# Kernel optimization log

Hardware: AMD Instinct MI355X
Metric: run time of the kernel (lower is better)

## Reference

```python
import jax, jax.numpy as jnp
import numpy as np

SEQ, B = 1024, 16384

def setup_inputs() -> dict:
    key = jax.random.key(0)
    ks = jax.random.split(key, 8)
    inputs = jax.random.normal(ks[0], (SEQ, B, 1), dtype=jnp.float32)
    returns = jax.random.uniform(ks[1], (SEQ - 1, B, 1), dtype=jnp.float32) * 0.02 - 0.01
    target = jax.random.uniform(ks[2], (1,), dtype=jnp.float32)  # pi_bar (no-trade region center)
    w_in = jax.random.normal(ks[3], (1, 1), dtype=jnp.float32)   # rnn.input_param.weight (1x1)
    w_h = jax.random.normal(ks[4], (1, 1), dtype=jnp.float32)    # rnn.hidden_param.weight (1x1)
    b_h = jax.random.normal(ks[5], (1, 1), dtype=jnp.float32)    # rnn.hidden_param.bias (1x1)
    w_fc1 = jax.random.normal(ks[6], (1, 1), dtype=jnp.float32)  # rnn.fc1_param.weight (1x1)
    w_fc2 = jax.random.normal(ks[7], (1, 1), dtype=jnp.float32)  # rnn.fc2_param.weight (1x1)
    return {"inputs": inputs, "returns": returns, "target": target,
            "w_in": w_in, "w_h": w_h, "b_h": b_h, "w_fc1": w_fc1, "w_fc2": w_fc2}


def reference(inputs, returns, target, w_in, w_h, b_h, w_fc1, w_fc2):
    # inputs: [S, B, 1], returns: [S-1, B, 1]; hidden_size == 1 so per-step state h: [B, 1]
    pi_bar = target[0]

    def step(h, xr):
        x, r = xr  # x: [B,1] input at step i, r: [B,1] return at step i-1
        # wealth renormalization of previous position
        h_adj = h * (1.0 + r) / (1.0 + h * r)
        # NoTradeRegionRNN.recurrence (all params are 1x1 -> scalar broadcasts)
        ingate = x @ w_in.T + w_h * h_adj - (pi_bar - b_h)
        ingate2 = w_fc1 * jax.nn.relu(ingate) + 2.0 * b_h
        h_new = w_fc2 * jax.nn.relu(ingate2) + pi_bar + b_h
        return h_new, h_new

    h0 = inputs[0]  # i==0: hidden = input[0] * ones -> just input[0], shape [B,1]
    hT, outs = jax.lax.scan(step, h0, (inputs[1:], returns))
    output = jnp.concatenate([h0[None], outs], axis=0)  # [S, B, 1]
    return output, hT
```

## Files before the change

### kernel.cpp

```cpp
#include <hip/hip_runtime.h>
#include <cstdint>


#define S_LEN 1024
#define B_LEN 16384
#define GSTEP ((size_t)4 * B_LEN)

typedef uint32_t u32x4 __attribute__((ext_vector_type(4)));
typedef float    f32x4 __attribute__((ext_vector_type(4)));
typedef float    f32x2 __attribute__((ext_vector_type(2)));

__device__ __forceinline__ u32x4 make_srsrc(const void* p) {
    u32x4 r;
    uint64_t a = (uint64_t)p;
    r.x = (uint32_t)a;
    r.y = (uint32_t)(a >> 32);
    r.z = 0xFFFFFFFFu;
    r.w = 0x00020000u;
    return r;
}

#define SBAR0 __builtin_amdgcn_sched_barrier(0)
#define WAITV(N) do { asm volatile("s_waitcnt vmcnt(%0)" :: "n"(N)); SBAR0; } while (0)
#define LGKMN(N) do { asm volatile("s_waitcnt lgkmcnt(%0)" :: "n"(N)); SBAR0; } while (0)

__device__ __forceinline__ void dma16(const float* g, float* l) {
    __builtin_amdgcn_global_load_lds(
        (const __attribute__((address_space(1))) void*)g,
        (__attribute__((address_space(3))) void*)l, 16, 0, 0);
}

__device__ __forceinline__ float step_fn(float h, float x, float r,
                                         float win, float wh,
                                         float c1, float c2, float c3,
                                         float wf1, float wf2) {
    float inv   = __builtin_amdgcn_rcpf(fmaf(h, r, 1.0f));
    float h_adj = fmaf(h, r, h) * inv;
    float ingate = fmaf(wh, h_adj, fmaf(x, win, c1));
    float t  = fmaxf(ingate, 0.0f);
    float g2 = fmaf(wf1, t, c2);
    float t2 = fmaxf(g2, 0.0f);
    return fmaf(wf2, t2, c3);
}

struct Consts { float winwf1, whwf1, c1wf1c2, c2p, wf2, c3; };

template<bool POS>
__device__ __forceinline__ void step_fast(float& st, float& hv,
                                          float x, float r, const Consts& C) {
    float A1 = C.wf2 * r;
    float B1 = C.c3 * r;
    float w  = fmaf(C.whwf1, r, C.whwf1);
    float A2 = C.wf2 * w;
    float B2 = C.c3 * w;
    float KK = fmaf(x, C.winwf1, C.c1wf1c2);
    float u  = fmaf(A1, st, B1);
    float M  = fmaf(A2, st, B2);
    float q  = fmaf(u, u, 1.0f);
    float om = 1.0f - u;
    float p  = om * q;
    float Aa = fmaf(M, p, KK);
    if (POS) st = fmaxf(Aa, C.c2p);
    else     st = fminf(fmaxf(Aa, 0.0f), C.c2p);
    hv = fmaf(C.wf2, st, C.c3);
}

template<bool POS>
__device__ __forceinline__ void step_first(float& st, float& hv,
                                           float x, float r, float h0,
                                           const Consts& C) {
    float w  = fmaf(C.whwf1, r, C.whwf1);
    float KK = fmaf(x, C.winwf1, C.c1wf1c2);
    float u  = h0 * r;
    float M  = w * h0;
    float q  = fmaf(u, u, 1.0f);
    float om = 1.0f - u;
    float p  = om * q;
    float Aa = fmaf(M, p, KK);
    if (POS) st = fmaxf(Aa, C.c2p);
    else     st = fminf(fmaxf(Aa, 0.0f), C.c2p);
    hv = fmaf(C.wf2, st, C.c3);
}

struct Bank { f32x2 x01, x23, r01, r23; };

#define RDG(g_, BK) do { \
    uint32_t ax_ = rbase + (uint32_t)(((g_) & 31) * 2048); \
    uint32_t ar_ = ax_ + 1024u; \
    asm volatile("ds_read2_b32 %0, %1 offset0:0 offset1:64"    : "=v"((BK).x01) : "v"(ax_)); \
    asm volatile("ds_read2_b32 %0, %1 offset0:128 offset1:192" : "=v"((BK).x23) : "v"(ax_)); \
    asm volatile("ds_read2_b32 %0, %1 offset0:0 offset1:64"    : "=v"((BK).r01) : "v"(ar_)); \
    asm volatile("ds_read2_b32 %0, %1 offset0:128 offset1:192" : "=v"((BK).r23) : "v"(ar_)); \
} while (0)

#define STEPS4B(BK) do { \
    step_fast<POS>(st, hv0, (BK).x01.x, (BK).r01.x, C); \
    step_fast<POS>(st, hv1, (BK).x01.y, (BK).r01.y, C); \
    step_fast<POS>(st, hv2, (BK).x23.x, (BK).r23.x, C); \
    step_fast<POS>(st, hv3, (BK).x23.y, (BK).r23.y, C); \
} while (0)

#define WRG(WA_) do { \
    asm volatile("ds_write2_b32 %0, %1, %2 offset0:0 offset1:64"    :: "v"(WA_), "v"(hv0), "v"(hv1)); \
    asm volatile("ds_write2_b32 %0, %1, %2 offset0:128 offset1:192" :: "v"(WA_), "v"(hv2), "v"(hv3)); \
} while (0)

#define PHASE(gr_, BKR, LGN_, BKC, WOFF_) do { \
    RDG(gr_, BKR); \
    LGKMN(LGN_); \
    STEPS4B(BKC); \
    { uint32_t wa_ = wb + (WOFF_); WRG(wa_); } \
} while (0)

template<bool POS>
__device__ __forceinline__ void wave0_impl(
    const float* inputs, const float* returns,
    float pi_bar, float win, float wh, float bh, float wf1, float wf2,
    float* out, int b0, int lane, float* ringp, float* outbp)
{
    const int b = b0 + lane;
    const float c1 = bh - pi_bar;
    const float c2 = 2.0f * bh;
    const float c3 = pi_bar + bh;
    Consts C;
    C.winwf1  = win * wf1;
    C.whwf1   = wh * wf1;
    C.c1wf1c2 = fmaf(c1, wf1, c2);
    C.c2p     = fmaxf(c2, 0.0f);
    C.wf2     = wf2;
    C.c3      = c3;

    const float h0v = inputs[b];
    out[b] = h0v;

    const uint32_t rbase = (uint32_t)(uintptr_t)ringp + (uint32_t)lane * 4u;
    const uint32_t wbase = (uint32_t)(uintptr_t)outbp + (uint32_t)lane * 4u;

    asm volatile("" ::: "memory");
    __builtin_amdgcn_s_barrier();

    Bank B0, B1, B2, B3;
    float st = 0.0f, hv0, hv1, hv2, hv3;

    RDG(0, B0);
    RDG(1, B1);
    LGKMN(0);

    for (int bt = 0; bt < 31; ++bt) {
        const int g0 = 8 * bt;
        const uint32_t wb = wbase + (uint32_t)((bt & 1) << 13);
        RDG(g0 + 2, B2);
        LGKMN(12);
        if (bt == 0) { step_first<POS>(st, hv0, B0.x01.x, B0.r01.x, h0v, C); }
        else         { step_fast<POS>(st, hv0, B0.x01.x, B0.r01.x, C); }
        step_fast<POS>(st, hv1, B0.x01.y, B0.r01.y, C);
        step_fast<POS>(st, hv2, B0.x23.x, B0.r23.x, C);
        step_fast<POS>(st, hv3, B0.x23.y, B0.r23.y, C);
        { uint32_t wa_ = wb; WRG(wa_); }
        PHASE(g0 + 3, B3, 10, B1, 1024);
        PHASE(g0 + 4, B0, 12, B2, 2048);
        PHASE(g0 + 5, B1, 12, B3, 3072);
        PHASE(g0 + 6, B2, 12, B0, 4096);
        PHASE(g0 + 7, B3, 12, B1, 5120);
        PHASE(g0 + 8, B0, 12, B2, 6144);
        LGKMN(8);
        STEPS4B(B3);
        { uint32_t wa_ = wb + 7168u; WRG(wa_); }
        RDG(g0 + 9, B1);
        LGKMN(4);
        __builtin_amdgcn_s_barrier();
    }

    {
        const uint32_t wb = wbase + 8192u;
        PHASE(250, B2, 12, B0, 0);
        PHASE(251, B3, 10, B1, 1024);
        PHASE(252, B0, 12, B2, 2048);
        PHASE(253, B1, 12, B3, 3072);
        PHASE(254, B2, 12, B0, 4096);
        PHASE(254, B3, 12, B1, 5120);
        LGKMN(8);
        STEPS4B(B2);
        { uint32_t wa_ = wb + 6144u; WRG(wa_); }
        LGKMN(0);
        __builtin_amdgcn_s_barrier();
    }

    asm volatile("" ::: "memory");

    float h = hv3;
#pragma unroll
    for (int s = 1021; s < S_LEN; ++s) {
        const float x = inputs[(size_t)s * B_LEN + b];
        const float r = returns[(size_t)(s - 1) * B_LEN + b];
        h = step_fn(h, x, r, win, wh, c1, c2, c3, wf1, wf2);
        out[(size_t)s * B_LEN + b] = h;
    }
    out[(size_t)S_LEN * B_LEN + b] = h;
}

#define DMA_GROUP() do { \
    float* lb_ = &ringf[(size_t)(dmag & 31) * 512]; \
    dma16(gxw, lb_); dma16(grw, lb_ + 256); \
    gxw += GSTEP; grw += GSTEP; ++dmag; \
} while (0)

#define WDR8(LOFF_, O0,O1,O2,O3,O4,O5,O6,O7) do { \
    uint32_t a_ = oa + (LOFF_); \
    asm volatile("ds_read_b128 %0, %1 offset:0"    : "=v"(O0) : "v"(a_)); \
    asm volatile("ds_read_b128 %0, %1 offset:1024" : "=v"(O1) : "v"(a_)); \
    asm volatile("ds_read_b128 %0, %1 offset:2048" : "=v"(O2) : "v"(a_)); \
    asm volatile("ds_read_b128 %0, %1 offset:3072" : "=v"(O3) : "v"(a_)); \
    asm volatile("ds_read_b128 %0, %1 offset:4096" : "=v"(O4) : "v"(a_)); \
    asm volatile("ds_read_b128 %0, %1 offset:5120" : "=v"(O5) : "v"(a_)); \
    asm volatile("ds_read_b128 %0, %1 offset:6144" : "=v"(O6) : "v"(a_)); \
    asm volatile("ds_read_b128 %0, %1 offset:7168" : "=v"(O7) : "v"(a_)); \
} while (0)

#define BST(O_) do { \
    asm volatile("buffer_store_dwordx4 %0, %1, %2, %3 offen" \
                 :: "v"(O_), "v"(vo), "s"(ro), "s"(so_)); \
    so_ += (4u << 16); \
} while (0)

#define W1_ITER(k_, LOFF_, NDMA_, PREN_, ENDN_, DOEND_, O0,O1,O2,O3,O4,O5,O6,O7) do { \
    __builtin_amdgcn_s_barrier(); \
    for (int gi_ = 0; gi_ < (NDMA_); ++gi_) { DMA_GROUP(); } \
    asm volatile("s_waitcnt vmcnt(%0)" :: "n"(PREN_)); SBAR0; \
    asm volatile("" :: "v"(O0),"v"(O1),"v"(O2),"v"(O3),"v"(O4),"v"(O5),"v"(O6),"v"(O7)); \
    WDR8(LOFF_, O0,O1,O2,O3,O4,O5,O6,O7); \
    LGKMN(0); \
    { uint32_t so_ = ((uint32_t)(32 * ((k_) - 1) + 1)) << 16; \
      BST(O0); BST(O1); BST(O2); BST(O3); BST(O4); BST(O5); BST(O6); BST(O7); } \
    if (DOEND_) { asm volatile("s_waitcnt vmcnt(%0)" :: "n"(ENDN_)); SBAR0; } \
} while (0)

__global__ __launch_bounds__(128) void wealth_rnn_kernel(
    const float* __restrict__ inputs,
    const float* __restrict__ returns,
    const float* __restrict__ target,
    const float* __restrict__ w_in_p,
    const float* __restrict__ w_h_p,
    const float* __restrict__ b_h_p,
    const float* __restrict__ w_fc1_p,
    const float* __restrict__ w_fc2_p,
    float* __restrict__ out)
{
    __shared__ float ringf[32 * 512];
    __shared__ float outbf[2 * 8 * 256];

    const int tid  = threadIdx.x;
    const int lane = tid & 63;
    const int wid  = tid >> 6;
    const int b0   = blockIdx.x * 64;

    if (wid == 0) {
        const float pi_bar = target[0];
        const float win = w_in_p[0];
        const float wh  = w_h_p[0];
        const float bh  = b_h_p[0];
        const float wf1 = w_fc1_p[0];
        const float wf2 = w_fc2_p[0];
        if (wf1 >= 0.0f)
            wave0_impl<true >(inputs, returns, pi_bar, win, wh, bh, wf1, wf2,
                              out, b0, lane, &ringf[0], &outbf[0]);
        else
            wave0_impl<false>(inputs, returns, pi_bar, win, wh, bh, wf1, wf2,
                              out, b0, lane, &ringf[0], &outbf[0]);
    } else {
        const int j = lane;
        u32x4 ro = make_srsrc(out);
        const uint32_t vo = (uint32_t)((((j >> 4) * B_LEN) + b0 + (j & 15) * 4) * 4);
        const uint32_t oa = (uint32_t)(uintptr_t)&outbf[0]
                            + (uint32_t)((j >> 4) * 256 + (j & 15) * 16);

        const int lr = j >> 4;
        const int lc = (j & 15) * 4;
        const float* gxw = inputs  + (size_t)(1 + lr) * B_LEN + b0 + lc;
        const float* grw = returns + (size_t)lr       * B_LEN + b0 + lc;
        int dmag = 0;

        for (int gi = 0; gi < 24; ++gi) { DMA_GROUP(); }
        WAITV(28);
        __builtin_amdgcn_s_barrier();

        for (int gi = 0; gi < 8; ++gi) { DMA_GROUP(); }
        WAITV(28);

        f32x4 o0={0,0,0,0},o1={0,0,0,0},o2={0,0,0,0},o3={0,0,0,0},
              o4={0,0,0,0},o5={0,0,0,0},o6={0,0,0,0},o7={0,0,0,0};
        f32x4 p0={0,0,0,0},p1={0,0,0,0},p2={0,0,0,0},p3={0,0,0,0},
              p4={0,0,0,0},p5={0,0,0,0},p6={0,0,0,0},p7={0,0,0,0};

        for (int k2 = 0; k2 < 13; ++k2) {
            const int k = 1 + 2 * k2;
            W1_ITER(k,     0,    8, 40, 36, 1, o0,o1,o2,o3,o4,o5,o6,o7);
            W1_ITER(k + 1, 8192, 8, 40, 36, 1, p0,p1,p2,p3,p4,p5,p6,p7);
        }
        W1_ITER(27, 0,    8, 40, 36, 1, o0,o1,o2,o3,o4,o5,o6,o7);
        W1_ITER(28, 8192, 7, 38, 34, 1, p0,p1,p2,p3,p4,p5,p6,p7);
        W1_ITER(29, 0,    0, 22, 18, 1, o0,o1,o2,o3,o4,o5,o6,o7);
        W1_ITER(30, 8192, 0,  8, 16, 1, p0,p1,p2,p3,p4,p5,p6,p7);
        W1_ITER(31, 0,    0,  8,  0, 0, o0,o1,o2,o3,o4,o5,o6,o7);
        __builtin_amdgcn_s_barrier();

        WAITV(8);
        asm volatile("" :: "v"(p0),"v"(p1),"v"(p2),"v"(p3),"v"(p4),"v"(p5),"v"(p6));
        {
            uint32_t a_ = oa + 8192u;
            asm volatile("ds_read_b128 %0, %1 offset:0"    : "=v"(p0) : "v"(a_));
            asm volatile("ds_read_b128 %0, %1 offset:1024" : "=v"(p1) : "v"(a_));
            asm volatile("ds_read_b128 %0, %1 offset:2048" : "=v"(p2) : "v"(a_));
            asm volatile("ds_read_b128 %0, %1 offset:3072" : "=v"(p3) : "v"(a_));
            asm volatile("ds_read_b128 %0, %1 offset:4096" : "=v"(p4) : "v"(a_));
            asm volatile("ds_read_b128 %0, %1 offset:5120" : "=v"(p5) : "v"(a_));
            asm volatile("ds_read_b128 %0, %1 offset:6144" : "=v"(p6) : "v"(a_));
        }
        LGKMN(0);
        {
            uint32_t so_ = ((uint32_t)993) << 16;
            BST(p0); BST(p1); BST(p2); BST(p3); BST(p4); BST(p5); BST(p6);
        }
    }
}

extern "C" void kernel_launch(void* const* d_in, const int* in_sizes, int n_in,
                              void* d_out, int out_size, void* d_ws, size_t ws_size,
                              hipStream_t stream) {
    const float* inputs  = (const float*)d_in[0];
    const float* returns = (const float*)d_in[1];
    const float* target  = (const float*)d_in[2];
    const float* w_in    = (const float*)d_in[3];
    const float* w_h     = (const float*)d_in[4];
    const float* b_h     = (const float*)d_in[5];
    const float* w_fc1   = (const float*)d_in[6];
    const float* w_fc2   = (const float*)d_in[7];
    float* out = (float*)d_out;

    dim3 grid(B_LEN / 64);
    dim3 block(128);
    hipLaunchKernelGGL(wealth_rnn_kernel, grid, block, 0, stream,
                       inputs, returns, target, w_in, w_h, b_h, w_fc1, w_fc2, out);
}
```

Baseline: 43.69 us.

## Store outputs directly from compute wave and enlarge LDS input ring

The compute wave now writes each step's hidden values straight to global memory with per-lane buffer_store_dword. It no longer stages them in an LDS output buffer for the helper wave to read back and store as dwordx4. The helper wave becomes a pure DMA producer, and the input ring grows from 32 to 64 groups with 16-step phases between barriers. The aim is to remove the LDS round trip and halve the barrier count. The cost is many narrower stores issued from the latency-critical serial wave, plus a larger LDS footprint.

```diff
diff --git a/kernel.cpp b/kernel.cpp
--- a/kernel.cpp
+++ b/kernel.cpp
@@ -7,7 +7,6 @@
 #define GSTEP ((size_t)4 * B_LEN)
 
 typedef uint32_t u32x4 __attribute__((ext_vector_type(4)));
-typedef float    f32x4 __attribute__((ext_vector_type(4)));
 typedef float    f32x2 __attribute__((ext_vector_type(2)));
 
 __device__ __forceinline__ u32x4 make_srsrc(const void* p) {
@@ -84,39 +83,37 @@
 
 struct Bank { f32x2 x01, x23, r01, r23; };
 
-#define RDG(g_, BK) do { \
-    uint32_t ax_ = rbase + (uint32_t)(((g_) & 31) * 2048); \
-    uint32_t ar_ = ax_ + 1024u; \
-    asm volatile("ds_read2_b32 %0, %1 offset0:0 offset1:64"    : "=v"((BK).x01) : "v"(ax_)); \
-    asm volatile("ds_read2_b32 %0, %1 offset0:128 offset1:192" : "=v"((BK).x23) : "v"(ax_)); \
+#define RDGA(AX_, BK) do { \
+    uint32_t ar_ = (AX_) + 1024u; \
+    asm volatile("ds_read2_b32 %0, %1 offset0:0 offset1:64"    : "=v"((BK).x01) : "v"(AX_)); \
+    asm volatile("ds_read2_b32 %0, %1 offset0:128 offset1:192" : "=v"((BK).x23) : "v"(AX_)); \
     asm volatile("ds_read2_b32 %0, %1 offset0:0 offset1:64"    : "=v"((BK).r01) : "v"(ar_)); \
     asm volatile("ds_read2_b32 %0, %1 offset0:128 offset1:192" : "=v"((BK).r23) : "v"(ar_)); \
 } while (0)
 
-#define STEPS4B(BK) do { \
-    step_fast<POS>(st, hv0, (BK).x01.x, (BK).r01.x, C); \
-    step_fast<POS>(st, hv1, (BK).x01.y, (BK).r01.y, C); \
-    step_fast<POS>(st, hv2, (BK).x23.x, (BK).r23.x, C); \
-    step_fast<POS>(st, hv3, (BK).x23.y, (BK).r23.y, C); \
-} while (0)
-
-#define WRG(WA_) do { \
-    asm volatile("ds_write2_b32 %0, %1, %2 offset0:0 offset1:64"    :: "v"(WA_), "v"(hv0), "v"(hv1)); \
-    asm volatile("ds_write2_b32 %0, %1, %2 offset0:128 offset1:192" :: "v"(WA_), "v"(hv2), "v"(hv3)); \
-} while (0)
-
-#define PHASE(gr_, BKR, LGN_, BKC, WOFF_) do { \
-    RDG(gr_, BKR); \
-    LGKMN(LGN_); \
-    STEPS4B(BKC); \
-    { uint32_t wa_ = wb + (WOFF_); WRG(wa_); } \
+#define BSTROW(HV_, ROWC_) do { \
+    uint32_t so_ = sob + (uint32_t)((ROWC_) << 16); \
+    asm volatile("buffer_store_dword %0, %1, %2, %3 offen" \
+                 :: "v"(HV_), "v"(voff), "s"(ro), "s"(so_)); \
+} while (0)
+
+#define PH(p_, BKR, BKC) do { \
+    int gr_ = g0 + (p_) + 2; if (gr_ > 254) gr_ = 254; \
+    { uint32_t ra_ = rbase + (uint32_t)((gr_ & 63) * 2048); RDGA(ra_, BKR); } \
+    LGKMN(8); \
+    step_fast<POS>(st, hv0, (BKC).x01.x, (BKC).r01.x, C); \
+    step_fast<POS>(st, hv1, (BKC).x01.y, (BKC).r01.y, C); \
+    step_fast<POS>(st, hv2, (BKC).x23.x, (BKC).r23.x, C); \
+    step_fast<POS>(st, hv3, (BKC).x23.y, (BKC).r23.y, C); \
+    BSTROW(hv0, 4 * (p_) + 1); BSTROW(hv1, 4 * (p_) + 2); \
+    BSTROW(hv2, 4 * (p_) + 3); BSTROW(hv3, 4 * (p_) + 4); \
 } while (0)
 
 template<bool POS>
 __device__ __forceinline__ void wave0_impl(
     const float* inputs, const float* returns,
     float pi_bar, float win, float wh, float bh, float wf1, float wf2,
-    float* out, int b0, int lane, float* ringp, float* outbp)
+    float* out, int b0, int lane, float* ringp)
 {
     const int b = b0 + lane;
     const float c1 = bh - pi_bar;
@@ -133,8 +130,9 @@
     const float h0v = inputs[b];
     out[b] = h0v;
 
+    u32x4 ro = make_srsrc(out);
+    const uint32_t voff = (uint32_t)(b * 4);
     const uint32_t rbase = (uint32_t)(uintptr_t)ringp + (uint32_t)lane * 4u;
-    const uint32_t wbase = (uint32_t)(uintptr_t)outbp + (uint32_t)lane * 4u;
 
     asm volatile("" ::: "memory");
     __builtin_amdgcn_s_barrier();
@@ -142,50 +140,40 @@
     Bank B0, B1, B2, B3;
     float st = 0.0f, hv0, hv1, hv2, hv3;
 
-    RDG(0, B0);
-    RDG(1, B1);
+    { uint32_t ra_ = rbase;          RDGA(ra_, B0); }
+    { uint32_t ra_ = rbase + 2048u;  RDGA(ra_, B1); }
     LGKMN(0);
 
-    for (int bt = 0; bt < 31; ++bt) {
-        const int g0 = 8 * bt;
-        const uint32_t wb = wbase + (uint32_t)((bt & 1) << 13);
-        RDG(g0 + 2, B2);
-        LGKMN(12);
-        if (bt == 0) { step_first<POS>(st, hv0, B0.x01.x, B0.r01.x, h0v, C); }
-        else         { step_fast<POS>(st, hv0, B0.x01.x, B0.r01.x, C); }
-        step_fast<POS>(st, hv1, B0.x01.y, B0.r01.y, C);
-        step_fast<POS>(st, hv2, B0.x23.x, B0.r23.x, C);
-        step_fast<POS>(st, hv3, B0.x23.y, B0.r23.y, C);
-        { uint32_t wa_ = wb; WRG(wa_); }
-        PHASE(g0 + 3, B3, 10, B1, 1024);
-        PHASE(g0 + 4, B0, 12, B2, 2048);
-        PHASE(g0 + 5, B1, 12, B3, 3072);
-        PHASE(g0 + 6, B2, 12, B0, 4096);
-        PHASE(g0 + 7, B3, 12, B1, 5120);
-        PHASE(g0 + 8, B0, 12, B2, 6144);
-        LGKMN(8);
-        STEPS4B(B3);
-        { uint32_t wa_ = wb + 7168u; WRG(wa_); }
-        RDG(g0 + 9, B1);
-        LGKMN(4);
-        __builtin_amdgcn_s_barrier();
-    }
-
+    for (int bt = 0; bt < 15; ++bt) {
+        const int g0 = 16 * bt;
+        const uint32_t sob = (uint32_t)(64 * bt) << 16;
+        if (bt == 0) {
+            { uint32_t ra_ = rbase + (uint32_t)(((g0 + 2) & 63) * 2048); RDGA(ra_, B2); }
+            LGKMN(8);
+            step_first<POS>(st, hv0, B0.x01.x, B0.r01.x, h0v, C);
+            step_fast<POS>(st, hv1, B0.x01.y, B0.r01.y, C);
+            step_fast<POS>(st, hv2, B0.x23.x, B0.r23.x, C);
+            step_fast<POS>(st, hv3, B0.x23.y, B0.r23.y, C);
+            BSTROW(hv0, 1); BSTROW(hv1, 2); BSTROW(hv2, 3); BSTROW(hv3, 4);
+        } else {
+            PH(0, B2, B0);
+        }
+        PH(1,  B3, B1); PH(2,  B0, B2); PH(3,  B1, B3);
+        PH(4,  B2, B0); PH(5,  B3, B1); PH(6,  B0, B2); PH(7,  B1, B3);
+        PH(8,  B2, B0); PH(9,  B3, B1); PH(10, B0, B2); PH(11, B1, B3);
+        PH(12, B2, B0); PH(13, B3, B1); PH(14, B0, B2); PH(15, B1, B3);
+        __builtin_amdgcn_s_barrier();
+    }
     {
-        const uint32_t wb = wbase + 8192u;
-        PHASE(250, B2, 12, B0, 0);
-        PHASE(251, B3, 10, B1, 1024);
-        PHASE(252, B0, 12, B2, 2048);
-        PHASE(253, B1, 12, B3, 3072);
-        PHASE(254, B2, 12, B0, 4096);
-        PHASE(254, B3, 12, B1, 5120);
-        LGKMN(8);
-        STEPS4B(B2);
-        { uint32_t wa_ = wb + 6144u; WRG(wa_); }
-        LGKMN(0);
-        __builtin_amdgcn_s_barrier();
-    }
-
+        const int g0 = 240;
+        const uint32_t sob = (uint32_t)(960) << 16;
+        PH(0,  B2, B0); PH(1,  B3, B1); PH(2,  B0, B2); PH(3,  B1, B3);
+        PH(4,  B2, B0); PH(5,  B3, B1); PH(6,  B0, B2); PH(7,  B1, B3);
+        PH(8,  B2, B0); PH(9,  B3, B1); PH(10, B0, B2); PH(11, B1, B3);
+        PH(12, B2, B0); PH(13, B3, B1); PH(14, B0, B2);
+        __builtin_amdgcn_s_barrier();
+    }
+    LGKMN(0);
     asm volatile("" ::: "memory");
 
     float h = hv3;
@@ -197,42 +185,14 @@
         out[(size_t)s * B_LEN + b] = h;
     }
     out[(size_t)S_LEN * B_LEN + b] = h;
+
+    WAITV(0);
 }
 
 #define DMA_GROUP() do { \
-    float* lb_ = &ringf[(size_t)(dmag & 31) * 512]; \
+    float* lb_ = &ringf[(size_t)(dmag & 63) * 512]; \
     dma16(gxw, lb_); dma16(grw, lb_ + 256); \
     gxw += GSTEP; grw += GSTEP; ++dmag; \
-} while (0)
-
-#define WDR8(LOFF_, O0,O1,O2,O3,O4,O5,O6,O7) do { \
-    uint32_t a_ = oa + (LOFF_); \
-    asm volatile("ds_read_b128 %0, %1 offset:0"    : "=v"(O0) : "v"(a_)); \
-    asm volatile("ds_read_b128 %0, %1 offset:1024" : "=v"(O1) : "v"(a_)); \
-    asm volatile("ds_read_b128 %0, %1 offset:2048" : "=v"(O2) : "v"(a_)); \
-    asm volatile("ds_read_b128 %0, %1 offset:3072" : "=v"(O3) : "v"(a_)); \
-    asm volatile("ds_read_b128 %0, %1 offset:4096" : "=v"(O4) : "v"(a_)); \
-    asm volatile("ds_read_b128 %0, %1 offset:5120" : "=v"(O5) : "v"(a_)); \
-    asm volatile("ds_read_b128 %0, %1 offset:6144" : "=v"(O6) : "v"(a_)); \
-    asm volatile("ds_read_b128 %0, %1 offset:7168" : "=v"(O7) : "v"(a_)); \
-} while (0)
-
-#define BST(O_) do { \
-    asm volatile("buffer_store_dwordx4 %0, %1, %2, %3 offen" \
-                 :: "v"(O_), "v"(vo), "s"(ro), "s"(so_)); \
-    so_ += (4u << 16); \
-} while (0)
-
-#define W1_ITER(k_, LOFF_, NDMA_, PREN_, ENDN_, DOEND_, O0,O1,O2,O3,O4,O5,O6,O7) do { \
-    __builtin_amdgcn_s_barrier(); \
-    for (int gi_ = 0; gi_ < (NDMA_); ++gi_) { DMA_GROUP(); } \
-    asm volatile("s_waitcnt vmcnt(%0)" :: "n"(PREN_)); SBAR0; \
-    asm volatile("" :: "v"(O0),"v"(O1),"v"(O2),"v"(O3),"v"(O4),"v"(O5),"v"(O6),"v"(O7)); \
-    WDR8(LOFF_, O0,O1,O2,O3,O4,O5,O6,O7); \
-    LGKMN(0); \
-    { uint32_t so_ = ((uint32_t)(32 * ((k_) - 1) + 1)) << 16; \
-      BST(O0); BST(O1); BST(O2); BST(O3); BST(O4); BST(O5); BST(O6); BST(O7); } \
-    if (DOEND_) { asm volatile("s_waitcnt vmcnt(%0)" :: "n"(ENDN_)); SBAR0; } \
 } while (0)
 
 __global__ __launch_bounds__(128) void wealth_rnn_kernel(
@@ -246,8 +206,7 @@
     const float* __restrict__ w_fc2_p,
     float* __restrict__ out)
 {
-    __shared__ float ringf[32 * 512];
-    __shared__ float outbf[2 * 8 * 256];
+    __shared__ float ringf[64 * 512];
 
     const int tid  = threadIdx.x;
     const int lane = tid & 63;
@@ -263,64 +222,33 @@
         const float wf2 = w_fc2_p[0];
         if (wf1 >= 0.0f)
             wave0_impl<true >(inputs, returns, pi_bar, win, wh, bh, wf1, wf2,
-                              out, b0, lane, &ringf[0], &outbf[0]);
+                              out, b0, lane, &ringf[0]);
         else
             wave0_impl<false>(inputs, returns, pi_bar, win, wh, bh, wf1, wf2,
-                              out, b0, lane, &ringf[0], &outbf[0]);
+                              out, b0, lane, &ringf[0]);
     } else {
         const int j = lane;
-        u32x4 ro = make_srsrc(out);
-        const uint32_t vo = (uint32_t)((((j >> 4) * B_LEN) + b0 + (j & 15) * 4) * 4);
-        const uint32_t oa = (uint32_t)(uintptr_t)&outbf[0]
-                            + (uint32_t)((j >> 4) * 256 + (j & 15) * 16);
-
         const int lr = j >> 4;
         const int lc = (j & 15) * 4;
         const float* gxw = inputs  + (size_t)(1 + lr) * B_LEN + b0 + lc;
         const float* grw = returns + (size_t)lr       * B_LEN + b0 + lc;
         int dmag = 0;
 
-        for (int gi = 0; gi < 24; ++gi) { DMA_GROUP(); }
+        for (int gi = 0; gi < 32; ++gi) { DMA_GROUP(); }
         WAITV(28);
         __builtin_amdgcn_s_barrier();
 
-        for (int gi = 0; gi < 8; ++gi) { DMA_GROUP(); }
-        WAITV(28);
-
-        f32x4 o0={0,0,0,0},o1={0,0,0,0},o2={0,0,0,0},o3={0,0,0,0},
-              o4={0,0,0,0},o5={0,0,0,0},o6={0,0,0,0},o7={0,0,0,0};
-        f32x4 p0={0,0,0,0},p1={0,0,0,0},p2={0,0,0,0},p3={0,0,0,0},
-              p4={0,0,0,0},p5={0,0,0,0},p6={0,0,0,0},p7={0,0,0,0};
-
-        for (int k2 = 0; k2 < 13; ++k2) {
-            const int k = 1 + 2 * k2;
-            W1_ITER(k,     0,    8, 40, 36, 1, o0,o1,o2,o3,o4,o5,o6,o7);
-            W1_ITER(k + 1, 8192, 8, 40, 36, 1, p0,p1,p2,p3,p4,p5,p6,p7);
+        for (int k = 0; k < 13; ++k) {
+            for (int gi = 0; gi < 16; ++gi) { DMA_GROUP(); }
+            WAITV(28);
+            __builtin_amdgcn_s_barrier();
         }
-        W1_ITER(27, 0,    8, 40, 36, 1, o0,o1,o2,o3,o4,o5,o6,o7);
-        W1_ITER(28, 8192, 7, 38, 34, 1, p0,p1,p2,p3,p4,p5,p6,p7);
-        W1_ITER(29, 0,    0, 22, 18, 1, o0,o1,o2,o3,o4,o5,o6,o7);
-        W1_ITER(30, 8192, 0,  8, 16, 1, p0,p1,p2,p3,p4,p5,p6,p7);
-        W1_ITER(31, 0,    0,  8,  0, 0, o0,o1,o2,o3,o4,o5,o6,o7);
-        __builtin_amdgcn_s_barrier();
-
-        WAITV(8);
-        asm volatile("" :: "v"(p0),"v"(p1),"v"(p2),"v"(p3),"v"(p4),"v"(p5),"v"(p6));
-        {
-            uint32_t a_ = oa + 8192u;
-            asm volatile("ds_read_b128 %0, %1 offset:0"    : "=v"(p0) : "v"(a_));
-            asm volatile("ds_read_b128 %0, %1 offset:1024" : "=v"(p1) : "v"(a_));
-            asm volatile("ds_read_b128 %0, %1 offset:2048" : "=v"(p2) : "v"(a_));
-            asm volatile("ds_read_b128 %0, %1 offset:3072" : "=v"(p3) : "v"(a_));
-            asm volatile("ds_read_b128 %0, %1 offset:4096" : "=v"(p4) : "v"(a_));
-            asm volatile("ds_read_b128 %0, %1 offset:5120" : "=v"(p5) : "v"(a_));
-            asm volatile("ds_read_b128 %0, %1 offset:6144" : "=v"(p6) : "v"(a_));
-        }
-        LGKMN(0);
-        {
-            uint32_t so_ = ((uint32_t)993) << 16;
-            BST(p0); BST(p1); BST(p2); BST(p3); BST(p4); BST(p5); BST(p6);
-        }
+        for (int gi = 0; gi < 15; ++gi) { DMA_GROUP(); }
+        WAITV(26);
+        __builtin_amdgcn_s_barrier();
+        WAITV(0);
+        __builtin_amdgcn_s_barrier();
+        __builtin_amdgcn_s_barrier();
     }
 }
 
```

Result: slower. 48.37 us (+10.7%).
